# Optimization experiments

Hardware: AMD Instinct MI355X
Metric: run time of the kernel (lower is better)

## Reference

```python
import jax, jax.numpy as jnp
import numpy as np

B, A, D, H, NL, DFF, V, NB = 32, 256, 512, 8, 6, 2048, 1000, 4
EMB = D // 8  # per-subtoken embedding dim, 8 subtokens concat to d_model


def setup_inputs() -> dict:
    key = jax.random.key(0)
    ks = jax.random.split(key, 10)
    s = 0.02
    p = {}
    p["src"] = jax.random.randint(ks[0], (B, A, 8), 0, V, dtype=jnp.int32)
    p["mask"] = jnp.ones((B, 1, A), dtype=bool)
    p["max_atoms"] = A
    # sinusoidal positional encoding table [A, D]
    pos = np.arange(A, dtype=np.float32)[:, None]
    div = np.power(10000.0, np.arange(0, D, 2, dtype=np.float32) / D)
    pe = np.zeros((A, D), dtype=np.float32)
    pe[:, 0::2] = np.sin(pos / div)
    pe[:, 1::2] = np.cos(pos / div)
    p["pe"] = jnp.asarray(pe)
    p["embed"] = s * jax.random.normal(ks[1], (V, EMB), dtype=jnp.float32)
    p["Wq"] = s * jax.random.normal(ks[2], (NL, D, D), dtype=jnp.float32)
    p["Wk"] = s * jax.random.normal(ks[3], (NL, D, D), dtype=jnp.float32)
    p["Wv"] = s * jax.random.normal(ks[4], (NL, D, D), dtype=jnp.float32)
    p["Wo"] = s * jax.random.normal(ks[5], (NL, D, D), dtype=jnp.float32)
    p["W1"] = s * jax.random.normal(ks[6], (NL, D, DFF), dtype=jnp.float32)
    p["W2"] = s * jax.random.normal(ks[7], (NL, DFF, D), dtype=jnp.float32)
    p["Wfl"] = s * jax.random.normal(ks[8], (2 * D, NB), dtype=jnp.float32)
    for n, sh in [("bq", (NL, D)), ("bk", (NL, D)), ("bv", (NL, D)), ("bo", (NL, D)),
                  ("b1", (NL, DFF)), ("b2", (NL, D)), ("ln1_b", (NL, D)), ("ln2_b", (NL, D)),
                  ("fn_b", (D,)), ("bfl", (NB,))]:
        p[n] = jnp.zeros(sh, dtype=jnp.float32)
    for n, sh in [("ln1_a", (NL, D)), ("ln2_a", (NL, D)), ("fn_a", (D,))]:
        p[n] = jnp.ones(sh, dtype=jnp.float32)
    return p


def _norm(x, a, b):
    # custom Norm: alpha * (x - mean) / (std_unbiased + eps) + bias
    mu = x.mean(-1, keepdims=True)
    sd = jnp.std(x, axis=-1, ddof=1, keepdims=True)
    return a * (x - mu) / (sd + 1e-6) + b


def _forward(src, mask, max_atoms, embed, pe, Wq, bq, Wk, bk, Wv, bv, Wo, bo,
             ln1_a, ln1_b, ln2_a, ln2_b, W1, b1, W2, b2, fn_a, fn_b, Wfl, bfl):
    b, L = src.shape[0], src.shape[1]
    x = embed[src].reshape(b, L, -1)  # [B, A, D]
    d = x.shape[-1]
    x = x * jnp.sqrt(jnp.float32(d)) + pe[None, :L]
    dk = d // H
    addm = jnp.where(mask[:, None, :, :], 0.0, -1e9)  # [B,1,1,A]
    for i in range(NL):
        # pre-norm self-attention + residual
        x2 = _norm(x, ln1_a[i], ln1_b[i])
        q = (x2 @ Wq[i] + bq[i]).reshape(b, L, H, dk)
        k = (x2 @ Wk[i] + bk[i]).reshape(b, L, H, dk)
        v = (x2 @ Wv[i] + bv[i]).reshape(b, L, H, dk)
        sc = jnp.einsum('bqhd,bkhd->bhqk', q, k) / jnp.sqrt(jnp.float32(dk)) + addm
        att = jax.nn.softmax(sc, axis=-1)
        o = jnp.einsum('bhqk,bkhd->bqhd', att, v).reshape(b, L, d)
        x = x + (o @ Wo[i] + bo[i])
        # pre-norm FFN + residual
        x2 = _norm(x, ln2_a[i], ln2_b[i])
        x = x + (jax.nn.relu(x2 @ W1[i] + b1[i]) @ W2[i] + b2[i])
    h = _norm(x, fn_a, fn_b)  # [B, A, D]
    # EdgeClassify: all-pairs concat(h_i, h_j) @ Wfl + bfl, computed without
    # materializing the [B, A, A, 2D] tensor (linearity of the Linear layer)
    left = h @ Wfl[:d]    # [B, A, NB]
    right = h @ Wfl[d:]   # [B, A, NB]
    return left[:, :, None, :] + right[:, None, :, :] + bfl  # [B, A, A, NB]


def reference(src, mask, max_atoms, pe, embed, Wq, Wk, Wv, Wo, W1, W2, Wfl,
              bq, bk, bv, bo, b1, b2, ln1_b, ln2_b, fn_b, bfl, ln1_a, ln2_a, fn_a):
    return _forward(src, mask, max_atoms, embed, pe, Wq, bq, Wk, bk, Wv, bv, Wo, bo,
                    ln1_a, ln1_b, ln2_a, ln2_b, W1, b1, W2, b2, fn_a, fn_b, Wfl, bfl)
```

## Files before the change

kernel.cpp:

```cpp
#include <hip/hip_runtime.h>
#include <hip/hip_bf16.h>

#define BB 32
#define AA 256
#define DD 512
#define HH 8
#define NLAYER 6
#define DFF 2048
#define NB 4

typedef float  f32x4_t  __attribute__((ext_vector_type(4)));
typedef short  bf16x8_t __attribute__((ext_vector_type(8)));

struct __align__(16) US8 { ushort u[8]; };

__device__ __forceinline__ ushort f2bf(float f) {
    __hip_bfloat16 h = __float2bfloat16(f);
    return *reinterpret_cast<ushort*>(&h);
}
__device__ __forceinline__ float bf2f(ushort u) {
    __hip_bfloat16 h;
    *reinterpret_cast<ushort*>(&h) = u;
    return __bfloat162float(h);
}

__device__ __forceinline__ void gload16(const void* g, void* l) {
    __builtin_amdgcn_global_load_lds(
        (const __attribute__((address_space(1))) void*)g,
        (__attribute__((address_space(3))) void*)l, 16, 0, 0);
}

__global__ __launch_bounds__(256) void embed_pe_kernel(
    const int* __restrict__ src, const float* __restrict__ embed,
    const float* __restrict__ pe, float* __restrict__ x)
{
    int t = blockIdx.x * 256 + threadIdx.x;
    int d4 = t & 127;
    int row = t >> 7;
    int a = row & 255;
    int d = d4 * 4;
    int sub = d >> 6;
    int e = d & 63;
    int tok = src[row * 8 + sub];
    float4 em = *(const float4*)&embed[tok * 64 + e];
    float4 p  = *(const float4*)&pe[a * DD + d];
    const float s = 22.627416997969522f;
    float4 r;
    r.x = em.x * s + p.x; r.y = em.y * s + p.y;
    r.z = em.z * s + p.z; r.w = em.w * s + p.w;
    *(float4*)&x[(long long)row * DD + d] = r;
}

template<bool OB>
__global__ __launch_bounds__(256) void layernorm512_kernel(
    const float* x, const float* __restrict__ alpha,
    const float* __restrict__ beta, void* yv)
{
    const int row = blockIdx.x * 4 + (threadIdx.x >> 6);
    const int lane = threadIdx.x & 63;
    const float* xr = x + (long long)row * DD;
    float4 v0 = *(const float4*)&xr[lane * 8];
    float4 v1 = *(const float4*)&xr[lane * 8 + 4];
    float s  = v0.x + v0.y + v0.z + v0.w + v1.x + v1.y + v1.z + v1.w;
    float ss = v0.x*v0.x + v0.y*v0.y + v0.z*v0.z + v0.w*v0.w
             + v1.x*v1.x + v1.y*v1.y + v1.z*v1.z + v1.w*v1.w;
    #pragma unroll
    for (int off = 1; off < 64; off <<= 1) {
        s  += __shfl_xor(s, off, 64);
        ss += __shfl_xor(ss, off, 64);
    }
    float mu = s * (1.0f / 512.0f);
    float var = fmaxf(ss - 512.0f * mu * mu, 0.0f) * (1.0f / 511.0f);
    float inv = 1.0f / (sqrtf(var) + 1e-6f);
    float4 a0 = *(const float4*)&alpha[lane * 8];
    float4 a1 = *(const float4*)&alpha[lane * 8 + 4];
    float4 b0 = *(const float4*)&beta[lane * 8];
    float4 b1 = *(const float4*)&beta[lane * 8 + 4];
    float o0 = a0.x * (v0.x - mu) * inv + b0.x;
    float o1 = a0.y * (v0.y - mu) * inv + b0.y;
    float o2 = a0.z * (v0.z - mu) * inv + b0.z;
    float o3 = a0.w * (v0.w - mu) * inv + b0.w;
    float o4 = a1.x * (v1.x - mu) * inv + b1.x;
    float o5 = a1.y * (v1.y - mu) * inv + b1.y;
    float o6 = a1.z * (v1.z - mu) * inv + b1.z;
    float o7 = a1.w * (v1.w - mu) * inv + b1.w;
    if (OB) {
        US8 o;
        o.u[0] = f2bf(o0); o.u[1] = f2bf(o1); o.u[2] = f2bf(o2); o.u[3] = f2bf(o3);
        o.u[4] = f2bf(o4); o.u[5] = f2bf(o5); o.u[6] = f2bf(o6); o.u[7] = f2bf(o7);
        *(US8*)((ushort*)yv + (long long)row * DD + lane * 8) = o;
    } else {
        float* yr = (float*)yv + (long long)row * DD + lane * 8;
        float4 w0 = {o0, o1, o2, o3}, w1 = {o4, o5, o6, o7};
        *(float4*)yr = w0;
        *(float4*)(yr + 4) = w1;
    }
}

__global__ __launch_bounds__(256) void wtrans_kernel(
    const float* __restrict__ src, ushort* __restrict__ dst,
    int Nsz, int Ksz, long long sSrc, long long sDst)
{
    __shared__ float tile[64][65];
    src += blockIdx.z * sSrc;
    dst += blockIdx.z * sDst;
    const int n0 = blockIdx.x * 64, k0 = blockIdx.y * 64;
    const int t = threadIdx.x, col = t & 63, r4 = t >> 6;
    #pragma unroll
    for (int p = 0; p < 16; ++p) {
        int row = p * 4 + r4;
        tile[row][col] = src[(long long)(k0 + row) * Nsz + n0 + col];
    }
    __syncthreads();
    #pragma unroll
    for (int p = 0; p < 16; ++p) {
        int row = p * 4 + r4;
        dst[(long long)(n0 + row) * Ksz + k0 + col] = f2bf(tile[col][row]);
    }
}

__global__ __launch_bounds__(256) void wtrans4_kernel(
    const float* __restrict__ Wq, const float* __restrict__ Wk,
    const float* __restrict__ Wv, const float* __restrict__ Wo,
    ushort* __restrict__ Wqkvt, ushort* __restrict__ Wot)
{
    __shared__ float tile[64][65];
    const int z = blockIdx.z, layer = z >> 2, mat = z & 3;
    const float* src = (mat == 0 ? Wq : mat == 1 ? Wk : mat == 2 ? Wv : Wo)
                     + (long long)layer * 262144;
    ushort* dst = (mat < 3)
        ? Wqkvt + (long long)layer * 786432 + (long long)mat * 262144
        : Wot + (long long)layer * 262144;
    const int n0 = blockIdx.x * 64, k0 = blockIdx.y * 64;
    const int t = threadIdx.x, col = t & 63, r4 = t >> 6;
    #pragma unroll
    for (int p = 0; p < 16; ++p) {
        int row = p * 4 + r4;
        tile[row][col] = src[(long long)(k0 + row) * 512 + n0 + col];
    }
    __syncthreads();
    #pragma unroll
    for (int p = 0; p < 16; ++p) {
        int row = p * 4 + r4;
        dst[(long long)(n0 + row) * 512 + k0 + col] = f2bf(tile[col][row]);
    }
}

__global__ void concat_bias_kernel(const float* __restrict__ bq,
    const float* __restrict__ bk, const float* __restrict__ bv,
    float* __restrict__ o)
{
    int i = blockIdx.x * 256 + threadIdx.x;
    if (i >= NLAYER * 1536) return;
    int l = i / 1536, r = i % 1536;
    float v = r < 512 ? bq[l * 512 + r]
            : (r < 1024 ? bk[l * 512 + r - 512] : bv[l * 512 + r - 1024]);
    o[i] = v;
}

__global__ __launch_bounds__(512, 4) void attn_kernel(
    const ushort* __restrict__ qk, const ushort* __restrict__ vT,
    ushort* __restrict__ Ob)
{
    __shared__ ushort Kl[256 * 64];
    __shared__ ushort Vl[64 * 256];
    __shared__ ushort Pl[8 * 16 * 64];

    const int t = threadIdx.x;
    const int bh = blockIdx.x;
    const int b = bh >> 3, h = bh & 7;
    const int w = t >> 6, lane = t & 63;
    const int lr = lane & 15, lg = lane >> 4;

    {
        const int j = t >> 3, slot = t & 7;
        const int chunk = slot ^ (j & 7);
        const ushort* srcK = qk + (long long)(b * 256 + j) * 1024 + 512 + h * 64 + chunk * 8;
        const int c = t >> 5, slv = t & 31;
        const int chv = slv ^ (c & 7);
        const ushort* srcV = vT + (long long)b * 131072 + (long long)(h * 64 + c) * 256 + chv * 8;
        #pragma unroll
        for (int r = 0; r < 4; ++r) {
            gload16(srcK + (long long)r * 64 * 1024, &Kl[(t + r * 512) * 8]);
            gload16(srcV + (long long)r * 16 * 256,  &Vl[(t + r * 512) * 8]);
        }
    }
    asm volatile("s_waitcnt vmcnt(0)" ::: "memory");
    __builtin_amdgcn_sched_barrier(0);
    __builtin_amdgcn_s_barrier();
    __builtin_amdgcn_sched_barrier(0);

    char* Pw = (char*)Pl + w * 2048;
    const char* Kc = (const char*)Kl;
    const char* Vc = (const char*)Vl;

    #pragma unroll 1
    for (int pass = 0; pass < 2; ++pass) {
        const int i0 = pass * 128 + w * 16;
        const ushort* qbase = qk + (long long)(b * 256 + i0 + lr) * 1024 + h * 64 + lg * 8;
        bf16x8_t qf0 = *(const bf16x8_t*)qbase;
        bf16x8_t qf1 = *(const bf16x8_t*)(qbase + 32);

        f32x4_t s[16];
        #pragma unroll
        for (int jf = 0; jf < 16; ++jf) s[jf] = (f32x4_t){0.f, 0.f, 0.f, 0.f};
        #pragma unroll
        for (int jf = 0; jf < 16; ++jf) {
            const int row = jf * 16 + lr;
            bf16x8_t k0 = *(const bf16x8_t*)(Kc + row * 128 + ((lg ^ (row & 7)) * 16));
            s[jf] = __builtin_amdgcn_mfma_f32_16x16x32_bf16(k0, qf0, s[jf], 0, 0, 0);
        }
        #pragma unroll
        for (int jf = 0; jf < 16; ++jf) {
            const int row = jf * 16 + lr;
            bf16x8_t k1 = *(const bf16x8_t*)(Kc + row * 128 + (((4 + lg) ^ (row & 7)) * 16));
            s[jf] = __builtin_amdgcn_mfma_f32_16x16x32_bf16(k1, qf1, s[jf], 0, 0, 0);
        }

        float m = -3.0e38f;
        #pragma unroll
        for (int jf = 0; jf < 16; ++jf)
            #pragma unroll
            for (int r = 0; r < 4; ++r) m = fmaxf(m, s[jf][r]);
        m = fmaxf(m, __shfl_xor(m, 16, 64));
        m = fmaxf(m, __shfl_xor(m, 32, 64));
        float l = 0.f;
        #pragma unroll
        for (int jf = 0; jf < 16; ++jf)
            #pragma unroll
            for (int r = 0; r < 4; ++r) {
                float e = __expf((s[jf][r] - m) * 0.125f);
                s[jf][r] = e; l += e;
            }
        l += __shfl_xor(l, 16, 64);
        l += __shfl_xor(l, 32, 64);
        const float inv = 1.0f / l;

        f32x4_t o[4];
        #pragma unroll
        for (int cf = 0; cf < 4; ++cf) o[cf] = (f32x4_t){0.f, 0.f, 0.f, 0.f};
        #pragma unroll
        for (int jq = 0; jq < 4; ++jq) {
            asm volatile("s_waitcnt lgkmcnt(0)" ::: "memory");
            __builtin_amdgcn_sched_barrier(0);
            #pragma unroll
            for (int jf4 = 0; jf4 < 4; ++jf4) {
                const int jf = jq * 4 + jf4;
                ushort4 u;
                u.x = f2bf(s[jf][0] * inv); u.y = f2bf(s[jf][1] * inv);
                u.z = f2bf(s[jf][2] * inv); u.w = f2bf(s[jf][3] * inv);
                const int off = (lr * 128 + jf4 * 32 + lg * 8) ^ ((lr & 7) << 4);
                *(ushort4*)(Pw + off) = u;
            }
            asm volatile("s_waitcnt lgkmcnt(0)" ::: "memory");
            __builtin_amdgcn_sched_barrier(0);
            #pragma unroll
            for (int ks2 = 0; ks2 < 2; ++ks2) {
                const int ks = jq * 2 + ks2;
                bf16x8_t pa = *(const bf16x8_t*)(Pw +
                    ((lr * 128 + ks2 * 64 + lg * 16) ^ ((lr & 7) << 4)));
                #pragma unroll
                for (int cf = 0; cf < 4; ++cf) {
                    const int crow = cf * 16 + lr;
                    bf16x8_t vb = *(const bf16x8_t*)(Vc + crow * 512 +
                        (((ks * 4 + lg) ^ (crow & 7)) * 16));
                    o[cf] = __builtin_amdgcn_mfma_f32_16x16x32_bf16(pa, vb, o[cf], 0, 0, 0);
                }
            }
        }
        asm volatile("s_waitcnt lgkmcnt(0)" ::: "memory");
        __builtin_amdgcn_sched_barrier(0);

        #pragma unroll
        for (int cf = 0; cf < 4; ++cf) {
            const int c = cf * 16 + lr;
            #pragma unroll
            for (int r = 0; r < 4; ++r) {
                const int i = i0 + lg * 4 + r;
                Ob[(long long)(b * 256 + i) * 512 + h * 64 + c] = f2bf(o[cf][r]);
            }
        }
    }
}

template<int BMt, int BNt, int BKt, int NT, int OUT, bool RELU, bool SWZ>
__global__ __launch_bounds__(256, 4) void gemm_nar(
    const ushort* __restrict__ A, const ushort* __restrict__ B,
    const float* __restrict__ bias, const float* __restrict__ res,
    void* __restrict__ Cv, ushort* __restrict__ C2,
    int lda, int ldb, int ldc, int gx)
{
    constexpr int SL  = BKt / 8;
    constexpr int RPI = 2048 / BKt;
    constexpr int AI  = BMt / RPI;
    constexpr int BI  = BNt / RPI;
    constexpr int HM = BMt / 2, HN = BNt / 2;
    constexpr int RM = HM / 16, RN = HN / 16;

    __shared__ ushort As[BMt * BKt];
    __shared__ ushort Bs[BNt * BKt];

    const int t = threadIdx.x;
    int nb, mb;
    if (SWZ) {
        const int nwg = gridDim.x, bid = blockIdx.x;
        const int swz = (bid & 7) * (nwg >> 3) + (bid >> 3);
        nb = swz % gx; mb = swz / gx;
    } else {
        nb = blockIdx.x; mb = blockIdx.y;
    }
    const int m0 = mb * BMt, n0 = nb * BNt;

    const int trow  = t / SL;
    const int tslot = (t % SL) ^ (trow & 7);
    const ushort* Ap = A + (long long)(m0 + trow) * lda + tslot * 8;
    const ushort* Bp = B + (long long)(n0 + trow) * ldb + tslot * 8;

    const int w = t >> 6, lane = t & 63;
    const int wr = w >> 1, wc = w & 1;
    const int lr = lane & 15, lg = lane >> 4;
    const int sx = lr & 7;

    f32x4_t acc[RM][RN];
    #pragma unroll
    for (int i = 0; i < RM; ++i)
        #pragma unroll
        for (int j = 0; j < RN; ++j)
            acc[i][j] = (f32x4_t){0.f, 0.f, 0.f, 0.f};

    for (int kt = 0; kt < NT; ++kt) {
        const long long ko = (long long)kt * BKt;
        #pragma unroll
        for (int i = 0; i < AI; ++i)
            gload16(Ap + ko + (long long)i * RPI * lda, &As[t * 8 + i * 2048]);
        #pragma unroll
        for (int i = 0; i < BI; ++i)
            gload16(Bp + ko + (long long)i * RPI * ldb, &Bs[t * 8 + i * 2048]);
        __syncthreads();

        #pragma unroll
        for (int kk = 0; kk < BKt / 32; ++kk) {
            bf16x8_t af[RM], bfr[RN];
            #pragma unroll
            for (int mf = 0; mf < RM; ++mf)
                af[mf] = *(const bf16x8_t*)
                    &As[(wr * HM + mf * 16 + lr) * BKt + (((kk * 4 + lg) ^ sx) * 8)];
            #pragma unroll
            for (int nf = 0; nf < RN; ++nf)
                bfr[nf] = *(const bf16x8_t*)
                    &Bs[(wc * HN + nf * 16 + lr) * BKt + (((kk * 4 + lg) ^ sx) * 8)];
            #pragma unroll
            for (int mf = 0; mf < RM; ++mf)
                #pragma unroll
                for (int nf = 0; nf < RN; ++nf)
                    acc[mf][nf] = __builtin_amdgcn_mfma_f32_16x16x32_bf16(
                        af[mf], bfr[nf], acc[mf][nf], 0, 0, 0);
        }
        __syncthreads();
    }

    #pragma unroll
    for (int nf = 0; nf < RN; ++nf) {
        const int col = n0 + wc * HN + nf * 16 + lr;
        const float bv = bias[col];
        #pragma unroll
        for (int mf = 0; mf < RM; ++mf) {
            const int row0 = m0 + wr * HM + mf * 16 + lg * 4;
            #pragma unroll
            for (int j = 0; j < 4; ++j) {
                float vv = acc[mf][nf][j] + bv;
                if (RELU) vv = fmaxf(vv, 0.0f);
                const int row = row0 + j;
                if (OUT == 0) {
                    ((ushort*)Cv)[(long long)row * ldc + col] = f2bf(vv);
                } else if (OUT == 1) {
                    const long long idx = (long long)row * ldc + col;
                    ((float*)Cv)[idx] = vv + res[idx];
                } else {
                    if (col < 1024) {
                        ((ushort*)Cv)[(long long)row * 1024 + col] = f2bf(vv);
                    } else {
                        const int bq_ = row >> 8, a_ = row & 255;
                        C2[(long long)bq_ * 131072 + (long long)(col - 1024) * 256 + a_] = f2bf(vv);
                    }
                }
            }
        }
    }
}

__global__ __launch_bounds__(256) void ln_edge_kernel(
    const float* __restrict__ x, const float* __restrict__ alpha,
    const float* __restrict__ beta, const float* __restrict__ Wfl,
    float* __restrict__ L, float* __restrict__ R)
{
    const int row = blockIdx.x * 4 + (threadIdx.x >> 6);
    const int lane = threadIdx.x & 63;
    const float* xr = x + (long long)row * DD;
    float4 v0 = *(const float4*)&xr[lane * 8];
    float4 v1 = *(const float4*)&xr[lane * 8 + 4];
    float s  = v0.x + v0.y + v0.z + v0.w + v1.x + v1.y + v1.z + v1.w;
    float ss = v0.x*v0.x + v0.y*v0.y + v0.z*v0.z + v0.w*v0.w
             + v1.x*v1.x + v1.y*v1.y + v1.z*v1.z + v1.w*v1.w;
    #pragma unroll
    for (int off = 1; off < 64; off <<= 1) {
        s  += __shfl_xor(s, off, 64);
        ss += __shfl_xor(ss, off, 64);
    }
    float mu = s * (1.0f / 512.0f);
    float var = fmaxf(ss - 512.0f * mu * mu, 0.0f) * (1.0f / 511.0f);
    float inv = 1.0f / (sqrtf(var) + 1e-6f);

    float h[8];
    {
        float4 a0 = *(const float4*)&alpha[lane * 8];
        float4 a1 = *(const float4*)&alpha[lane * 8 + 4];
        float4 b0 = *(const float4*)&beta[lane * 8];
        float4 b1 = *(const float4*)&beta[lane * 8 + 4];
        h[0] = a0.x * (v0.x - mu) * inv + b0.x;
        h[1] = a0.y * (v0.y - mu) * inv + b0.y;
        h[2] = a0.z * (v0.z - mu) * inv + b0.z;
        h[3] = a0.w * (v0.w - mu) * inv + b0.w;
        h[4] = a1.x * (v1.x - mu) * inv + b1.x;
        h[5] = a1.y * (v1.y - mu) * inv + b1.y;
        h[6] = a1.z * (v1.z - mu) * inv + b1.z;
        h[7] = a1.w * (v1.w - mu) * inv + b1.w;
    }
    float accL[NB] = {}, accR[NB] = {};
    #pragma unroll
    for (int tt = 0; tt < 8; ++tt) {
        const int e = lane * 8 + tt;
        float4 wl = *(const float4*)&Wfl[e * NB];
        float4 wr = *(const float4*)&Wfl[(DD + e) * NB];
        accL[0] = fmaf(h[tt], wl.x, accL[0]);
        accL[1] = fmaf(h[tt], wl.y, accL[1]);
        accL[2] = fmaf(h[tt], wl.z, accL[2]);
        accL[3] = fmaf(h[tt], wl.w, accL[3]);
        accR[0] = fmaf(h[tt], wr.x, accR[0]);
        accR[1] = fmaf(h[tt], wr.y, accR[1]);
        accR[2] = fmaf(h[tt], wr.z, accR[2]);
        accR[3] = fmaf(h[tt], wr.w, accR[3]);
    }
    #pragma unroll
    for (int n = 0; n < NB; ++n) {
        #pragma unroll
        for (int off = 1; off < 64; off <<= 1) {
            accL[n] += __shfl_xor(accL[n], off, 64);
            accR[n] += __shfl_xor(accR[n], off, 64);
        }
    }
    if (lane == 0) {
        #pragma unroll
        for (int n = 0; n < NB; ++n) {
            L[row * NB + n] = accL[n];
            R[row * NB + n] = accR[n];
        }
    }
}

__global__ __launch_bounds__(256) void edge_combine_kernel(
    const float* __restrict__ L, const float* __restrict__ R,
    const float* __restrict__ bfl, float* __restrict__ out)
{
    int idx = blockIdx.x * 256 + threadIdx.x;
    int j = idx & 255;
    int bi = idx >> 8;
    int b = bi >> 8;
    float4 l = *(const float4*)&L[bi * NB];
    float4 r = *(const float4*)&R[(b * 256 + j) * NB];
    float4 bf = *(const float4*)bfl;
    float4 o;
    o.x = l.x + r.x + bf.x; o.y = l.y + r.y + bf.y;
    o.z = l.z + r.z + bf.z; o.w = l.w + r.w + bf.w;
    *(float4*)&out[(long long)idx * NB] = o;
}

extern "C" void kernel_launch(void* const* d_in, const int* in_sizes, int n_in,
                              void* d_out, int out_size, void* d_ws, size_t ws_size,
                              hipStream_t stream)
{
    const int*   src   = (const int*)  d_in[0];
    const float* pe    = (const float*)d_in[3];
    const float* emb   = (const float*)d_in[4];
    const float* Wq    = (const float*)d_in[5];
    const float* Wk    = (const float*)d_in[6];
    const float* Wv    = (const float*)d_in[7];
    const float* Wo    = (const float*)d_in[8];
    const float* W1    = (const float*)d_in[9];
    const float* W2    = (const float*)d_in[10];
    const float* Wfl   = (const float*)d_in[11];
    const float* bq    = (const float*)d_in[12];
    const float* bk    = (const float*)d_in[13];
    const float* bv    = (const float*)d_in[14];
    const float* bo    = (const float*)d_in[15];
    const float* b1    = (const float*)d_in[16];
    const float* b2    = (const float*)d_in[17];
    const float* ln1_b = (const float*)d_in[18];
    const float* ln2_b = (const float*)d_in[19];
    const float* fn_b  = (const float*)d_in[20];
    const float* bfl   = (const float*)d_in[21];
    const float* ln1_a = (const float*)d_in[22];
    const float* ln2_a = (const float*)d_in[23];
    const float* fn_a  = (const float*)d_in[24];
    float* out = (float*)d_out;

    const long long ROWS = (long long)BB * AA;
    char* p = (char*)d_ws;
    float*  x    = (float*)p;  p += ROWS * DD * 4;
    ushort* x2b  = (ushort*)p; p += ROWS * DD * 2;
    ushort* qk   = (ushort*)p;
    ushort* h1   = qk;
    p += ROWS * 1024 * 2;
    ushort* vT   = (ushort*)p; p += (long long)BB * DD * AA * 2;
    p += 8 * 1024 * 1024;
    ushort* Wqkvt= (ushort*)p; p += (long long)NLAYER * 1536 * 512 * 2;
    ushort* Wot  = (ushort*)p; p += (long long)NLAYER * 512 * 512 * 2;
    ushort* W1t  = (ushort*)p; p += (long long)NLAYER * 2048 * 512 * 2;
    ushort* W2t  = (ushort*)p; p += (long long)NLAYER * 512 * 2048 * 2;
    float*  bqkv = (float*)p;  p += (long long)NLAYER * 1536 * 4;
    float*  left = (float*)p;  p += ROWS * NB * 4;
    float*  right= (float*)p;  p += ROWS * NB * 4;

    wtrans4_kernel<<<dim3(8, 8, 24), 256, 0, stream>>>(Wq, Wk, Wv, Wo, Wqkvt, Wot);
    wtrans_kernel<<<dim3(32, 8, 6), 256, 0, stream>>>(W1, W1t, 2048, 512,  1048576LL, 1048576LL);
    wtrans_kernel<<<dim3(8, 32, 6), 256, 0, stream>>>(W2, W2t, 512,  2048, 1048576LL, 1048576LL);
    concat_bias_kernel<<<36, 256, 0, stream>>>(bq, bk, bv, bqkv);

    embed_pe_kernel<<<4096, 256, 0, stream>>>(src, emb, pe, x);

    for (int i = 0; i < NLAYER; ++i) {
        layernorm512_kernel<true><<<2048, 256, 0, stream>>>(
            x, ln1_a + i * DD, ln1_b + i * DD, x2b);
        gemm_nar<128, 128, 64, 8, 2, false, true><<<768, 256, 0, stream>>>(
            x2b, Wqkvt + (long long)i * 786432, bqkv + i * 1536, nullptr,
            qk, vT, 512, 512, 1024, 12);
        attn_kernel<<<256, 512, 0, stream>>>(qk, vT, x2b);
        gemm_nar<128, 64, 64, 8, 1, false, true><<<512, 256, 0, stream>>>(
            x2b, Wot + (long long)i * 262144, bo + i * DD, x,
            x, nullptr, 512, 512, 512, 8);
        layernorm512_kernel<true><<<2048, 256, 0, stream>>>(
            x, ln2_a + i * DD, ln2_b + i * DD, x2b);
        gemm_nar<128, 128, 64, 8, 0, true, true><<<1024, 256, 0, stream>>>(
            x2b, W1t + (long long)i * 1048576, b1 + i * DFF, nullptr,
            h1, nullptr, 512, 512, 2048, 16);
        gemm_nar<64, 64, 128, 16, 1, false, true><<<1024, 256, 0, stream>>>(
            h1, W2t + (long long)i * 1048576, b2 + i * DD, x,
            x, nullptr, 2048, 2048, 512, 8);
    }

    ln_edge_kernel<<<2048, 256, 0, stream>>>(x, fn_a, fn_b, Wfl, left, right);
    edge_combine_kernel<<<8192, 256, 0, stream>>>(left, right, bfl, out);
}
```

Before: 699.6 us.

## Add 256x256 eight-wave pipelined GEMM for QKV and FFN1 projections

Adds a new GEMM kernel with 256x256 output tiles, 512 threads (8 waves) and double-buffered LDS with direct global-to-LDS loads. Each K-tile is split into four quarter-phases that interleave the next tile's loads with MFMA work, using explicit vmcnt waits, barriers and setprio. The QKV and W1 projections switch to it, cutting block counts (192 and 256) and raising per-block data reuse. In exchange, occupancy is lower, 64 KB of LDS is used per block and there are many barriers, and with only 256 CUs the grids may leave some CUs idle or poorly load-balanced.

Measured after the change: 1.232 ms. 1.76x slower.

```diff
diff --git a/kernel.cpp b/kernel.cpp
--- a/kernel.cpp
+++ b/kernel.cpp
@@ -1,5 +1,6 @@
 #include <hip/hip_runtime.h>
 #include <hip/hip_bf16.h>
+#include <type_traits>
 
 #define BB 32
 #define AA 256
@@ -29,6 +30,13 @@
         (const __attribute__((address_space(1))) void*)g,
         (__attribute__((address_space(3))) void*)l, 16, 0, 0);
 }
+
+template<int N> __device__ __forceinline__ void wait_vmcnt() {
+    if constexpr      (N == 0) asm volatile("s_waitcnt vmcnt(0)" ::: "memory");
+    else if constexpr (N == 2) asm volatile("s_waitcnt vmcnt(2)" ::: "memory");
+    else static_assert(N == 0, "add vmcnt literal");
+}
+template<int N> using ic = std::integral_constant<int, N>;
 
 __global__ __launch_bounds__(256) void embed_pe_kernel(
     const int* __restrict__ src, const float* __restrict__ embed,
@@ -283,6 +291,141 @@
     }
 }
 
+template<int NTK, int OUT, bool RELU>
+__global__ __launch_bounds__(512, 2) void gemm8p(
+    const ushort* __restrict__ A, const ushort* __restrict__ B,
+    const float* __restrict__ bias, void* __restrict__ Cv,
+    ushort* __restrict__ C2, int lda, int ldb, int ldc, int gn)
+{
+    __shared__ ushort As[2][256 * 64];
+    __shared__ ushort Bs[2][256 * 64];
+
+    const int t = threadIdx.x;
+    const int nwg = gridDim.x, bid = blockIdx.x;
+    const int swz = (bid & 7) * (nwg >> 3) + (bid >> 3);
+    const int nb = swz % gn, mb = swz / gn;
+    const int m0 = mb * 256, n0 = nb * 256;
+
+    const int trow = t >> 3;
+    const int tslot = (t & 7) ^ (trow & 7);
+    const ushort* Ap = A + (long long)(m0 + trow) * lda + tslot * 8;
+    const ushort* Bp = B + (long long)(n0 + trow) * ldb + tslot * 8;
+
+    const int w = t >> 6, lane = t & 63;
+    const int wr = w >> 2, wc = w & 3;
+    const int lr = lane & 15, lg = lane >> 4;
+
+    f32x4_t acc[8][4];
+    #pragma unroll
+    for (int i = 0; i < 8; ++i)
+        #pragma unroll
+        for (int j = 0; j < 4; ++j)
+            acc[i][j] = (f32x4_t){0.f, 0.f, 0.f, 0.f};
+
+    auto stage = [&](int kt, int ht) {
+        const int s = kt & 1;
+        const long long ko = (long long)kt * 64;
+        const int half = ht & 1;
+        const bool isA = ht < 2;
+        const int ld = isA ? lda : ldb;
+        ushort* dst = (isA ? &As[s][0] : &Bs[s][0]) + half * 8192 + t * 8;
+        const ushort* src = (isA ? Ap : Bp) + ko + (long long)(half * 128) * ld;
+        gload16(src, dst);
+        gload16(src + (long long)64 * ld, dst + 4096);
+    };
+
+    auto phase = [&](auto qc, int kt, int skt, int sht, auto wvc) {
+        constexpr int Q = decltype(qc)::value;
+        constexpr int WV = decltype(wvc)::value;
+        if (sht >= 0) stage(skt, sht);
+        if constexpr (WV >= 0) wait_vmcnt<WV>();
+        __builtin_amdgcn_sched_barrier(0);
+        __builtin_amdgcn_s_barrier();
+        __builtin_amdgcn_sched_barrier(0);
+        const int s = kt & 1;
+        constexpr int QM = Q >> 1, QN = Q & 1;
+        bf16x8_t af[4][2], bf[2][2];
+        #pragma unroll
+        for (int i = 0; i < 4; ++i) {
+            const int row = wr * 128 + (QM * 4 + i) * 16 + lr;
+            #pragma unroll
+            for (int ks = 0; ks < 2; ++ks)
+                af[i][ks] = *(const bf16x8_t*)
+                    &As[s][row * 64 + (((ks * 4 + lg) ^ (row & 7)) * 8)];
+        }
+        #pragma unroll
+        for (int j = 0; j < 2; ++j) {
+            const int row = wc * 64 + (QN * 2 + j) * 16 + lr;
+            #pragma unroll
+            for (int ks = 0; ks < 2; ++ks)
+                bf[j][ks] = *(const bf16x8_t*)
+                    &Bs[s][row * 64 + (((ks * 4 + lg) ^ (row & 7)) * 8)];
+        }
+        __builtin_amdgcn_s_setprio(1);
+        #pragma unroll
+        for (int i = 0; i < 4; ++i)
+            #pragma unroll
+            for (int j = 0; j < 2; ++j)
+                #pragma unroll
+                for (int ks = 0; ks < 2; ++ks)
+                    acc[QM * 4 + i][QN * 2 + j] = __builtin_amdgcn_mfma_f32_16x16x32_bf16(
+                        af[i][ks], bf[j][ks], acc[QM * 4 + i][QN * 2 + j], 0, 0, 0);
+        __builtin_amdgcn_s_setprio(0);
+        __builtin_amdgcn_sched_barrier(0);
+        __builtin_amdgcn_s_barrier();
+        __builtin_amdgcn_sched_barrier(0);
+    };
+
+    stage(0, 0); stage(0, 1); stage(0, 2); stage(0, 3);
+
+    #pragma unroll 1
+    for (int it = 0; it < NTK / 2; ++it) {
+        const int kt = 2 * it;
+        const bool last = (it == NTK / 2 - 1);
+        phase(ic<0>{}, kt, kt + 1, 0, ic<2>{});
+        phase(ic<1>{}, kt, kt + 1, 1, ic<-1>{});
+        phase(ic<2>{}, kt, kt + 1, 2, ic<-1>{});
+        phase(ic<3>{}, kt, kt + 1, 3, ic<-1>{});
+        if (last) {
+            phase(ic<0>{}, kt + 1, -1, -1, ic<0>{});
+            phase(ic<1>{}, kt + 1, -1, -1, ic<-1>{});
+            phase(ic<2>{}, kt + 1, -1, -1, ic<-1>{});
+            phase(ic<3>{}, kt + 1, -1, -1, ic<-1>{});
+        } else {
+            phase(ic<0>{}, kt + 1, kt + 2, 0, ic<2>{});
+            phase(ic<1>{}, kt + 1, kt + 2, 1, ic<-1>{});
+            phase(ic<2>{}, kt + 1, kt + 2, 2, ic<-1>{});
+            phase(ic<3>{}, kt + 1, kt + 2, 3, ic<-1>{});
+        }
+    }
+
+    #pragma unroll
+    for (int nf = 0; nf < 4; ++nf) {
+        const int col = n0 + wc * 64 + nf * 16 + lr;
+        const float bv = bias[col];
+        #pragma unroll
+        for (int mf = 0; mf < 8; ++mf) {
+            const int row0 = m0 + wr * 128 + mf * 16 + lg * 4;
+            #pragma unroll
+            for (int j = 0; j < 4; ++j) {
+                float vv = acc[mf][nf][j] + bv;
+                if (RELU) vv = fmaxf(vv, 0.0f);
+                const int row = row0 + j;
+                if (OUT == 0) {
+                    ((ushort*)Cv)[(long long)row * ldc + col] = f2bf(vv);
+                } else {
+                    if (col < 1024) {
+                        ((ushort*)Cv)[(long long)row * 1024 + col] = f2bf(vv);
+                    } else {
+                        const int bq_ = row >> 8, a_ = row & 255;
+                        C2[(long long)bq_ * 131072 + (long long)(col - 1024) * 256 + a_] = f2bf(vv);
+                    }
+                }
+            }
+        }
+    }
+}
+
 template<int BMt, int BNt, int BKt, int NT, int OUT, bool RELU, bool SWZ>
 __global__ __launch_bounds__(256, 4) void gemm_nar(
     const ushort* __restrict__ A, const ushort* __restrict__ B,
@@ -531,18 +674,18 @@
     for (int i = 0; i < NLAYER; ++i) {
         layernorm512_kernel<true><<<2048, 256, 0, stream>>>(
             x, ln1_a + i * DD, ln1_b + i * DD, x2b);
-        gemm_nar<128, 128, 64, 8, 2, false, true><<<768, 256, 0, stream>>>(
-            x2b, Wqkvt + (long long)i * 786432, bqkv + i * 1536, nullptr,
-            qk, vT, 512, 512, 1024, 12);
+        gemm8p<8, 2, false><<<192, 512, 0, stream>>>(
+            x2b, Wqkvt + (long long)i * 786432, bqkv + i * 1536,
+            qk, vT, 512, 512, 1024, 6);
         attn_kernel<<<256, 512, 0, stream>>>(qk, vT, x2b);
         gemm_nar<128, 64, 64, 8, 1, false, true><<<512, 256, 0, stream>>>(
             x2b, Wot + (long long)i * 262144, bo + i * DD, x,
             x, nullptr, 512, 512, 512, 8);
         layernorm512_kernel<true><<<2048, 256, 0, stream>>>(
             x, ln2_a + i * DD, ln2_b + i * DD, x2b);
-        gemm_nar<128, 128, 64, 8, 0, true, true><<<1024, 256, 0, stream>>>(
-            x2b, W1t + (long long)i * 1048576, b1 + i * DFF, nullptr,
-            h1, nullptr, 512, 512, 2048, 16);
+        gemm8p<8, 0, true><<<256, 512, 0, stream>>>(
+            x2b, W1t + (long long)i * 1048576, b1 + i * DFF,
+            h1, nullptr, 512, 512, 2048, 8);
         gemm_nar<64, 64, 128, 16, 1, false, true><<<1024, 256, 0, stream>>>(
             h1, W2t + (long long)i * 1048576, b2 + i * DD, x,
             x, nullptr, 2048, 2048, 512, 8);
```
